# Kernel tuning notes

Hardware: AMD Instinct MI355X
Metric: run time of the kernel (lower is better)

Reference implementation:

```python
import jax, jax.numpy as jnp
import numpy as np

D_MODEL = 768
NUM_HEADS = 12
HEAD_DIM = D_MODEL // NUM_HEADS  # 64, also rotary dim
INTERMEDIATE = 1152
WINDOW = 128          # config.local_attention (layer_id=1 -> local layer)
ROPE_BASE = 10000.0   # local_rope_theta
EPS = 1e-5


def layer_norm_nocenter(x, gamma):
    # keras LayerNormalization(center=False): mean-subtract, no beta
    mu = jnp.mean(x, axis=-1, keepdims=True)
    var = jnp.var(x, axis=-1, keepdims=True)
    return (x - mu) * jax.lax.rsqrt(var + EPS) * gamma


def rotate_half(x):
    x1, x2 = jnp.split(x, 2, axis=-1)
    return jnp.concatenate([-x2, x1], axis=-1)


def setup_inputs() -> dict:
    key = jax.random.key(0)
    ks = jax.random.split(key, 7)
    B, S = 4, 2048
    hidden_states = jax.random.normal(ks[0], (B, S, D_MODEL), dtype=jnp.float32)
    attention_mask = jnp.zeros((B, 1, S, S), dtype=jnp.float32)  # no padding
    s = 0.02
    attn_norm_gamma = jnp.ones((D_MODEL,), dtype=jnp.float32)
    wqkv = jax.random.normal(ks[1], (D_MODEL, 3 * D_MODEL), dtype=jnp.float32) * s
    wo_attn = jax.random.normal(ks[2], (D_MODEL, D_MODEL), dtype=jnp.float32) * s
    mlp_norm_gamma = jnp.ones((D_MODEL,), dtype=jnp.float32)
    wi = jax.random.normal(ks[3], (D_MODEL, 2 * INTERMEDIATE), dtype=jnp.float32) * s
    wo_mlp = jax.random.normal(ks[4], (INTERMEDIATE, D_MODEL), dtype=jnp.float32) * s
    return {
        'hidden_states': hidden_states,
        'attention_mask': attention_mask,
        'attn_norm_gamma': attn_norm_gamma,
        'wqkv': wqkv,
        'wo_attn': wo_attn,
        'mlp_norm_gamma': mlp_norm_gamma,
        'wi': wi,
        'wo_mlp': wo_mlp,
    }


def reference(hidden_states, attention_mask, attn_norm_gamma, wqkv, wo_attn,
              mlp_norm_gamma, wi, wo_mlp):
    B, S, Dm = hidden_states.shape
    H, Dh = NUM_HEADS, HEAD_DIM

    # RoPE cache (NTKScaling with scaling_factor=1 -> plain RoPE)
    idx = jnp.arange(0, Dh, 2, dtype=jnp.float32)
    inv_freq = 1.0 / (ROPE_BASE ** (idx / Dh))          # [Dh/2]
    t = jnp.arange(S, dtype=jnp.float32)
    freqs = t[:, None] * inv_freq[None, :]              # [S, Dh/2]
    emb = jnp.concatenate([freqs, freqs], axis=-1)      # [S, Dh]
    cos = jnp.cos(emb)[None, None]                      # [1,1,S,Dh]
    sin = jnp.sin(emb)[None, None]

    # combined sliding-window + padding mask
    pos = jnp.arange(S)
    dist = jnp.abs(pos[:, None] - pos[None, :])
    neg = jnp.finfo(jnp.float32).min
    local = jnp.where(dist <= WINDOW // 2, 0.0, neg).astype(jnp.float32)
    mask = attention_mask + local[None, None]           # [B,1,S,S]

    # attention (layer_id != 0 -> pre-norm)
    x = layer_norm_nocenter(hidden_states, attn_norm_gamma)
    qkv = (x @ wqkv).reshape(B, S, 3, H, Dh).transpose(2, 0, 3, 1, 4)
    q, k, v = qkv[0], qkv[1], qkv[2]                    # [B,H,S,Dh]
    q = q * cos + rotate_half(q) * sin
    k = k * cos + rotate_half(k) * sin

    scale = 1.0 / jnp.sqrt(jnp.asarray(Dh, q.dtype))
    scores = jnp.einsum('bhqd,bhkd->bhqk', q, k) * scale + mask
    attn = jax.nn.softmax(scores, axis=-1)
    ctx = jnp.einsum('bhqk,bhkd->bhqd', attn, v)
    attn_out = ctx.transpose(0, 2, 1, 3).reshape(B, S, Dm) @ wo_attn

    h = hidden_states + attn_out

    # GLU MLP: Wi -> split -> gelu(x)*gate -> Wo, residual
    n = layer_norm_nocenter(h, mlp_norm_gamma)
    x_in, gate = jnp.split(n @ wi, 2, axis=-1)
    mlp = jax.nn.gelu(x_in, approximate=False) * gate
    return h + mlp @ wo_mlp
```

## Files before the change

### kernel.cpp

```cpp
#include <hip/hip_runtime.h>
#include <cstdint>
#include <cstddef>

typedef __bf16 bf16;
typedef float f32x4 __attribute__((ext_vector_type(4)));
typedef __bf16 bf16x8 __attribute__((ext_vector_type(8)));
typedef __bf16 bf16x4 __attribute__((ext_vector_type(4)));

#define MFMA16(a, b, c) __builtin_amdgcn_mfma_f32_16x16x32_bf16((a), (b), (c), 0, 0, 0)

__device__ __forceinline__ void gload_lds16(const void* g, void* l) {
  __builtin_amdgcn_global_load_lds((__attribute__((address_space(1))) void*)g,
                                   (__attribute__((address_space(3))) void*)l,
                                   16, 0, 0);
}

__global__ __launch_bounds__(256) void wconv_kernel(const float* __restrict__ W,
                                                    bf16* __restrict__ Wt, int K, int N) {
  __shared__ float tile[32][33];
  const int n0 = blockIdx.x * 32, k0 = blockIdx.y * 32;
  const int t = threadIdx.x;
  const int c = t & 31, r = t >> 5;
#pragma unroll
  for (int i = 0; i < 4; ++i)
    tile[r + i * 8][c] = W[(size_t)(k0 + r + i * 8) * N + n0 + c];
  __syncthreads();
#pragma unroll
  for (int i = 0; i < 4; ++i)
    Wt[(size_t)(n0 + r + i * 8) * K + k0 + c] = (bf16)tile[c][r + i * 8];
}

__global__ __launch_bounds__(256) void ln_kernel(const float* __restrict__ X,
                                                 const float* __restrict__ gamma,
                                                 bf16* __restrict__ out) {
  const int row = blockIdx.x, t = threadIdx.x;
  const float* xr = X + (size_t)row * 768;
  float v0 = xr[t], v1 = xr[t + 256], v2 = xr[t + 512];
  float s = v0 + v1 + v2;
  float s2 = v0 * v0 + v1 * v1 + v2 * v2;
#pragma unroll
  for (int m = 1; m <= 32; m <<= 1) {
    s += __shfl_xor(s, m, 64);
    s2 += __shfl_xor(s2, m, 64);
  }
  __shared__ float red[8];
  const int w = t >> 6, lane = t & 63;
  if (lane == 0) { red[w] = s; red[4 + w] = s2; }
  __syncthreads();
  s = red[0] + red[1] + red[2] + red[3];
  s2 = red[4] + red[5] + red[6] + red[7];
  const float mu = s * (1.f / 768.f);
  const float var = s2 * (1.f / 768.f) - mu * mu;
  const float rs = rsqrtf(var + 1e-5f);
  out[(size_t)row * 768 + t] = (bf16)((v0 - mu) * rs * gamma[t]);
  out[(size_t)row * 768 + t + 256] = (bf16)((v1 - mu) * rs * gamma[t + 256]);
  out[(size_t)row * 768 + t + 512] = (bf16)((v2 - mu) * rs * gamma[t + 512]);
}

template <int BM, bool RES, typename TOUT>
__global__ __launch_bounds__(256) void gemm_bt(const bf16* __restrict__ A,
                                               const bf16* __restrict__ Bt,
                                               const float* __restrict__ Res,
                                               TOUT* __restrict__ C, int M, int N, int K) {
  constexpr int MT = BM / 32;
  __shared__ __align__(16) bf16 As[BM * 64];
  __shared__ __align__(16) bf16 Bs[128 * 64];
  const int t = threadIdx.x;
  const int lane = t & 63;
  const int w = t >> 6;
  const int wm = w >> 1, wn = w & 1;
  const int row0 = blockIdx.y * BM, col0 = blockIdx.x * 128;
  const int rm = lane & 15, qd = lane >> 4;
  f32x4 acc[MT][4] = {};
  for (int k0 = 0; k0 < K; k0 += 64) {
#pragma unroll
    for (int i = 0; i < BM / 32; ++i) {
      int c = i * 256 + t;
      int r = c >> 3, j = (c & 7) ^ (r & 7);
      gload_lds16(A + (size_t)(row0 + r) * K + (k0 + j * 8), &As[c * 8]);
    }
#pragma unroll
    for (int i = 0; i < 4; ++i) {
      int c = i * 256 + t;
      int r = c >> 3, j = (c & 7) ^ (r & 7);
      gload_lds16(Bt + (size_t)(col0 + r) * K + (k0 + j * 8), &Bs[c * 8]);
    }
    __syncthreads();
#pragma unroll
    for (int kb = 0; kb < 2; ++kb) {
      bf16x8 af[MT], bfr[4];
#pragma unroll
      for (int mt = 0; mt < MT; ++mt) {
        int r = wm * (MT * 16) + mt * 16 + rm;
        af[mt] = *(const bf16x8*)&As[r * 64 + (((kb * 4 + qd) ^ (r & 7)) * 8)];
      }
#pragma unroll
      for (int nt = 0; nt < 4; ++nt) {
        int r = wn * 64 + nt * 16 + rm;
        bfr[nt] = *(const bf16x8*)&Bs[r * 64 + (((kb * 4 + qd) ^ (r & 7)) * 8)];
      }
#pragma unroll
      for (int mt = 0; mt < MT; ++mt)
#pragma unroll
        for (int nt = 0; nt < 4; ++nt)
          acc[mt][nt] = MFMA16(af[mt], bfr[nt], acc[mt][nt]);
    }
    __syncthreads();
  }
#pragma unroll
  for (int mt = 0; mt < MT; ++mt)
#pragma unroll
    for (int nt = 0; nt < 4; ++nt) {
      const int gc = col0 + wn * 64 + nt * 16 + rm;
#pragma unroll
      for (int r = 0; r < 4; ++r) {
        const int gr = row0 + wm * (MT * 16) + mt * 16 + qd * 4 + r;
        float v = acc[mt][nt][r];
        const size_t idx = (size_t)gr * N + gc;
        if (RES) v += Res[idx];
        C[idx] = (TOUT)v;
      }
    }
}

__global__ __launch_bounds__(256) void gemm_qkv(const bf16* __restrict__ A,
                                                const bf16* __restrict__ Bt,
                                                bf16* __restrict__ Qb,
                                                bf16* __restrict__ Kb,
                                                bf16* __restrict__ Vt) {
  __shared__ __align__(16) bf16 As[128 * 64];
  __shared__ __align__(16) bf16 Bs[128 * 64];
  const int t = threadIdx.x;
  const int lane = t & 63;
  const int w = t >> 6;
  const int wm = w >> 1, wn = w & 1;
  const int row0 = blockIdx.y * 128, col0 = blockIdx.x * 128;
  const int rm = lane & 15, qd = lane >> 4;
  f32x4 acc[4][4] = {};
  for (int k0 = 0; k0 < 768; k0 += 64) {
#pragma unroll
    for (int i = 0; i < 4; ++i) {
      int c = i * 256 + t;
      int r = c >> 3, j = (c & 7) ^ (r & 7);
      gload_lds16(A + (size_t)(row0 + r) * 768 + (k0 + j * 8), &As[c * 8]);
      int c2 = i * 256 + t;
      gload_lds16(Bt + (size_t)(col0 + r) * 768 + (k0 + j * 8), &Bs[c2 * 8]);
    }
    __syncthreads();
#pragma unroll
    for (int kb = 0; kb < 2; ++kb) {
      bf16x8 af[4], bfr[4];
#pragma unroll
      for (int mt = 0; mt < 4; ++mt) {
        int r = wm * 64 + mt * 16 + rm;
        af[mt] = *(const bf16x8*)&As[r * 64 + (((kb * 4 + qd) ^ (r & 7)) * 8)];
      }
#pragma unroll
      for (int nt = 0; nt < 4; ++nt) {
        int r = wn * 64 + nt * 16 + rm;
        bfr[nt] = *(const bf16x8*)&Bs[r * 64 + (((kb * 4 + qd) ^ (r & 7)) * 8)];
      }
#pragma unroll
      for (int mt = 0; mt < 4; ++mt)
#pragma unroll
        for (int nt = 0; nt < 4; ++nt)
          acc[mt][nt] = MFMA16(af[mt], bfr[nt], acc[mt][nt]);
    }
    __syncthreads();
  }

  const int head_id = blockIdx.x * 2 + wn;
  const int typ = head_id / 12;
  const int h = head_id - typ * 12;
  const int b = row0 >> 11;
  const int sw = (row0 & 2047) + wm * 64;
  const size_t bhbase = (size_t)(b * 12 + h) * 2048;

  if (typ < 2) {
    bf16* dst = typ ? Kb : Qb;
    float invf[2];
#pragma unroll
    for (int nt = 0; nt < 2; ++nt)
      invf[nt] = exp2f((float)(nt * 16 + rm) * -0.41524101186092029f);
#pragma unroll
    for (int mt = 0; mt < 4; ++mt)
#pragma unroll
      for (int r = 0; r < 4; ++r) {
        int s = sw + mt * 16 + qd * 4 + r;
#pragma unroll
        for (int nt = 0; nt < 2; ++nt) {
          float ang = (float)s * invf[nt];
          float rev = ang * 0.15915494309189535f;
          rev -= floorf(rev);
          float sn = __builtin_amdgcn_sinf(rev);
          float cs = __builtin_amdgcn_cosf(rev);
          float x1 = acc[mt][nt][r], x2 = acc[mt][nt + 2][r];
          int d = nt * 16 + rm;
          dst[(bhbase + s) * 64 + d] = (bf16)(x1 * cs - x2 * sn);
          dst[(bhbase + s) * 64 + d + 32] = (bf16)(x2 * cs + x1 * sn);
        }
      }
  } else {
#pragma unroll
    for (int mt = 0; mt < 4; ++mt)
#pragma unroll
      for (int nt = 0; nt < 4; ++nt) {
        int d = nt * 16 + rm;
        int s4 = sw + mt * 16 + qd * 4;
        bf16x4 v4;
#pragma unroll
        for (int r = 0; r < 4; ++r) v4[r] = (bf16)acc[mt][nt][r];
        *(bf16x4*)&Vt[(bhbase * 64) + ((size_t)(h * 0) ) + ((size_t)( (b * 12 + h) * 64 + d)) * 2048 + s4 - bhbase * 64] = v4;
      }
  }
}

__global__ __launch_bounds__(256) void gemm_wi_geglu(const bf16* __restrict__ A,
                                                     const bf16* __restrict__ Bt,
                                                     bf16* __restrict__ outp) {
  __shared__ __align__(16) bf16 As[128 * 64];
  __shared__ __align__(16) bf16 Bxs[64 * 64];
  __shared__ __align__(16) bf16 Bgs[64 * 64];
  const int t = threadIdx.x;
  const int lane = t & 63;
  const int w = t >> 6;
  const int wm = w >> 1, wn = w & 1;
  const int row0 = blockIdx.y * 128, col0 = blockIdx.x * 64;
  const int rm = lane & 15, qd = lane >> 4;
  f32x4 accx[4][2] = {}, accg[4][2] = {};
  for (int k0 = 0; k0 < 768; k0 += 64) {
#pragma unroll
    for (int i = 0; i < 4; ++i) {
      int c = i * 256 + t;
      int r = c >> 3, j = (c & 7) ^ (r & 7);
      gload_lds16(A + (size_t)(row0 + r) * 768 + (k0 + j * 8), &As[c * 8]);
    }
#pragma unroll
    for (int i = 0; i < 2; ++i) {
      int c = i * 256 + t;
      int r = c >> 3, j = (c & 7) ^ (r & 7);
      gload_lds16(Bt + (size_t)(col0 + r) * 768 + (k0 + j * 8), &Bxs[c * 8]);
      gload_lds16(Bt + (size_t)(1152 + col0 + r) * 768 + (k0 + j * 8), &Bgs[c * 8]);
    }
    __syncthreads();
#pragma unroll
    for (int kb = 0; kb < 2; ++kb) {
      bf16x8 af[4], bx[2], bg[2];
#pragma unroll
      for (int mt = 0; mt < 4; ++mt) {
        int r = wm * 64 + mt * 16 + rm;
        af[mt] = *(const bf16x8*)&As[r * 64 + (((kb * 4 + qd) ^ (r & 7)) * 8)];
      }
#pragma unroll
      for (int nt = 0; nt < 2; ++nt) {
        int r = wn * 32 + nt * 16 + rm;
        int off = r * 64 + (((kb * 4 + qd) ^ (r & 7)) * 8);
        bx[nt] = *(const bf16x8*)&Bxs[off];
        bg[nt] = *(const bf16x8*)&Bgs[off];
      }
#pragma unroll
      for (int mt = 0; mt < 4; ++mt)
#pragma unroll
        for (int nt = 0; nt < 2; ++nt) {
          accx[mt][nt] = MFMA16(af[mt], bx[nt], accx[mt][nt]);
          accg[mt][nt] = MFMA16(af[mt], bg[nt], accg[mt][nt]);
        }
    }
    __syncthreads();
  }
#pragma unroll
  for (int mt = 0; mt < 4; ++mt)
#pragma unroll
    for (int nt = 0; nt < 2; ++nt) {
      const int gc = col0 + wn * 32 + nt * 16 + rm;
#pragma unroll
      for (int r = 0; r < 4; ++r) {
        const int gr = row0 + wm * 64 + mt * 16 + qd * 4 + r;
        float x = accx[mt][nt][r], g = accg[mt][nt][r];
        float ge = 0.5f * x * (1.0f + erff(x * 0.70710678118654752f));
        outp[(size_t)gr * 1152 + gc] = (bf16)(ge * g);
      }
    }
}

__global__ __launch_bounds__(256) void attn_kernel(const bf16* __restrict__ Qb,
                                                   const bf16* __restrict__ Kb,
                                                   const bf16* __restrict__ Vt,
                                                   const float* __restrict__ am,
                                                   bf16* __restrict__ ctx) {
  __shared__ __align__(16) bf16 KP[64 * 200];
  __shared__ __align__(16) bf16 Vts[64 * 192];
  bf16* Ks = KP;
  bf16* Ps = KP;

  const int t = threadIdx.x;
  const int lane = t & 63, w = t >> 6;
  const int rm = lane & 15, qd = lane >> 4;
  const int s0 = blockIdx.x * 64;
  const int bh = blockIdx.y;
  const int b = bh / 12, h = bh - b * 12;
  const size_t baseQ = (size_t)bh * 2048;

#pragma unroll
  for (int i = 0; i < 6; ++i) {
    int c = i * 256 + t;
    int r = c >> 3, j = (c & 7) ^ (r & 7);
    int key = min(max(s0 - 64 + r, 0), 2047);
    gload_lds16(Kb + (baseQ + key) * 64 + j * 8, &Ks[c * 8]);
  }
#pragma unroll
  for (int i = 0; i < 6; ++i) {
    int c = i * 256 + t;
    int r = c / 24, jl = c - r * 24;
    int j = (jl & 24) | ((jl & 7) ^ (r & 7));
    int k0 = min(max(s0 - 64 + j * 8, 0), 2040);
    gload_lds16(Vt + ((size_t)bh * 64 + r) * 2048 + k0, &Vts[c * 8]);
  }

  bf16x8 aq[2];
#pragma unroll
  for (int kb = 0; kb < 2; ++kb)
    aq[kb] = *(const bf16x8*)&Qb[(baseQ + s0 + w * 16 + rm) * 64 + kb * 32 + qd * 8];

  float msk[12][4];
#pragma unroll
  for (int nt = 0; nt < 12; ++nt) {
    int key = s0 - 64 + nt * 16 + rm;
#pragma unroll
    for (int r = 0; r < 4; ++r) {
      int qpos = s0 + w * 16 + qd * 4 + r;
      bool valid = (key >= 0) && (key < 2048) && (key - qpos <= 64) && (qpos - key <= 64);
      msk[nt][r] = valid ? am[((size_t)b * 2048 + qpos) * 2048 + key] : -3e38f;
    }
  }
  __syncthreads();

  f32x4 sc[12];
#pragma unroll
  for (int nt = 0; nt < 12; ++nt) {
    f32x4 a = {0.f, 0.f, 0.f, 0.f};
#pragma unroll
    for (int kb = 0; kb < 2; ++kb) {
      int r = nt * 16 + rm;
      bf16x8 bk = *(const bf16x8*)&Ks[r * 64 + (((kb * 4 + qd) ^ (rm & 7)) * 8)];
      a = MFMA16(aq[kb], bk, a);
    }
    sc[nt] = a;
  }

  float mx[4] = {-3e38f, -3e38f, -3e38f, -3e38f};
#pragma unroll
  for (int nt = 0; nt < 12; ++nt)
#pragma unroll
    for (int r = 0; r < 4; ++r) {
      float v = (msk[nt][r] <= -2.9e38f) ? -3e38f : sc[nt][r] * 0.125f + msk[nt][r];
      sc[nt][r] = v;
      mx[r] = fmaxf(mx[r], v);
    }
#pragma unroll
  for (int r = 0; r < 4; ++r)
#pragma unroll
    for (int m = 1; m <= 8; m <<= 1) mx[r] = fmaxf(mx[r], __shfl_xor(mx[r], m, 64));
  float sum[4] = {0.f, 0.f, 0.f, 0.f};
#pragma unroll
  for (int nt = 0; nt < 12; ++nt)
#pragma unroll
    for (int r = 0; r < 4; ++r) {
      float p = (sc[nt][r] > -1e37f) ? __expf(sc[nt][r] - mx[r]) : 0.f;
      sc[nt][r] = p;
      sum[r] += p;
    }
#pragma unroll
  for (int r = 0; r < 4; ++r)
#pragma unroll
    for (int m = 1; m <= 8; m <<= 1) sum[r] += __shfl_xor(sum[r], m, 64);
  float inv[4];
#pragma unroll
  for (int r = 0; r < 4; ++r) inv[r] = 1.f / sum[r];

  __syncthreads();

#pragma unroll
  for (int nt = 0; nt < 12; ++nt)
#pragma unroll
    for (int r = 0; r < 4; ++r)
      Ps[(w * 16 + qd * 4 + r) * 200 + nt * 16 + rm] = (bf16)(sc[nt][r] * inv[r]);

  f32x4 o[4] = {};
#pragma unroll
  for (int ks = 0; ks < 6; ++ks) {
    bf16x8 ap = *(const bf16x8*)&Ps[(w * 16 + rm) * 200 + ks * 32 + qd * 8];
#pragma unroll
    for (int nt = 0; nt < 4; ++nt) {
      int kc = ks * 4 + qd;
      bf16x8 bv = *(const bf16x8*)&Vts[(nt * 16 + rm) * 192 +
                                       (((kc & 24) | ((kc & 7) ^ (rm & 7))) * 8)];
      o[nt] = MFMA16(ap, bv, o[nt]);
    }
  }
#pragma unroll
  for (int nt = 0; nt < 4; ++nt)
#pragma unroll
    for (int r = 0; r < 4; ++r) {
      int q_ = s0 + w * 16 + qd * 4 + r;
      ctx[((size_t)(b * 2048 + q_)) * 768 + h * 64 + nt * 16 + rm] = (bf16)o[nt][r];
    }
}

extern "C" void kernel_launch(void* const* d_in, const int* in_sizes, int n_in,
                              void* d_out, int out_size, void* d_ws, size_t ws_size,
                              hipStream_t stream) {
  (void)in_sizes; (void)n_in; (void)out_size; (void)ws_size;
  const float* hidden = (const float*)d_in[0];
  const float* amask = (const float*)d_in[1];
  const float* g1 = (const float*)d_in[2];
  const float* wqkv = (const float*)d_in[3];
  const float* woa = (const float*)d_in[4];
  const float* g2 = (const float*)d_in[5];
  const float* wi = (const float*)d_in[6];
  const float* wom = (const float*)d_in[7];
  float* out = (float*)d_out;

  char* p = (char*)d_ws;
  size_t o = 0;
  auto take = [&](size_t bytes) {
    char* r = p + o;
    o = (o + bytes + 255) & ~(size_t)255;
    return r;
  };
  bf16* wqkvT = (bf16*)take((size_t)2304 * 768 * 2);
  bf16* woaT = (bf16*)take((size_t)768 * 768 * 2);
  bf16* wiT = (bf16*)take((size_t)2304 * 768 * 2);
  bf16* womT = (bf16*)take((size_t)768 * 1152 * 2);
  bf16* xn = (bf16*)take((size_t)8192 * 768 * 2);
  bf16* Qb = (bf16*)take((size_t)98304 * 64 * 2);
  bf16* Kb = (bf16*)take((size_t)98304 * 64 * 2);
  bf16* Vt = (bf16*)take((size_t)98304 * 64 * 2);
  bf16* ctxb = (bf16*)take((size_t)8192 * 768 * 2);
  float* hbuf = (float*)take((size_t)8192 * 768 * 4);
  bf16* mlp = (bf16*)take((size_t)8192 * 1152 * 2);

  wconv_kernel<<<dim3(72, 24), 256, 0, stream>>>(wqkv, wqkvT, 768, 2304);
  wconv_kernel<<<dim3(24, 24), 256, 0, stream>>>(woa, woaT, 768, 768);
  wconv_kernel<<<dim3(72, 24), 256, 0, stream>>>(wi, wiT, 768, 2304);
  wconv_kernel<<<dim3(24, 36), 256, 0, stream>>>(wom, womT, 1152, 768);

  ln_kernel<<<8192, 256, 0, stream>>>(hidden, g1, xn);
  gemm_qkv<<<dim3(18, 64), 256, 0, stream>>>(xn, wqkvT, Qb, Kb, Vt);
  attn_kernel<<<dim3(32, 48), 256, 0, stream>>>(Qb, Kb, Vt, amask, ctxb);
  gemm_bt<64, true, float><<<dim3(6, 128), 256, 0, stream>>>(ctxb, woaT, hidden, hbuf,
                                                             8192, 768, 768);

  ln_kernel<<<8192, 256, 0, stream>>>(hbuf, g2, xn);
  gemm_wi_geglu<<<dim3(18, 64), 256, 0, stream>>>(xn, wiT, mlp);
  gemm_bt<64, true, float><<<dim3(6, 128), 256, 0, stream>>>(mlp, womT, hbuf, out,
                                                             8192, 768, 1152);
}
```

Before: 329.5 us.

## Interleave Wi columns for GEGLU, stage V transpose via LDS, merge weight conversion

```diff
diff --git a/kernel.cpp b/kernel.cpp
--- a/kernel.cpp
+++ b/kernel.cpp
@@ -15,10 +15,26 @@
                                    16, 0, 0);
 }
 
-__global__ __launch_bounds__(256) void wconv_kernel(const float* __restrict__ W,
-                                                    bf16* __restrict__ Wt, int K, int N) {
+__global__ __launch_bounds__(256) void wconv_all(const float* __restrict__ wqkv,
+                                                 const float* __restrict__ woa,
+                                                 const float* __restrict__ wi,
+                                                 const float* __restrict__ wom,
+                                                 bf16* __restrict__ wqkvT,
+                                                 bf16* __restrict__ woaT,
+                                                 bf16* __restrict__ wiIT,
+                                                 bf16* __restrict__ womT) {
+  int id = blockIdx.x;
+  const float* W;
+  bf16* Wt;
+  int K, N, bx, by;
+  bool inter = false;
+  if (id < 1728) { W = wqkv; Wt = wqkvT; K = 768; N = 2304; bx = id % 72; by = id / 72; }
+  else if (id < 2304) { id -= 1728; W = woa; Wt = woaT; K = 768; N = 768; bx = id % 24; by = id / 24; }
+  else if (id < 4032) { id -= 2304; W = wi; Wt = wiIT; K = 768; N = 2304; inter = true; bx = id % 72; by = id / 72; }
+  else { id -= 4032; W = wom; Wt = womT; K = 1152; N = 768; bx = id % 24; by = id / 24; }
+
   __shared__ float tile[32][33];
-  const int n0 = blockIdx.x * 32, k0 = blockIdx.y * 32;
+  const int n0 = bx * 32, k0 = by * 32;
   const int t = threadIdx.x;
   const int c = t & 31, r = t >> 5;
 #pragma unroll
@@ -26,8 +42,11 @@
     tile[r + i * 8][c] = W[(size_t)(k0 + r + i * 8) * N + n0 + c];
   __syncthreads();
 #pragma unroll
-  for (int i = 0; i < 4; ++i)
-    Wt[(size_t)(n0 + r + i * 8) * K + k0 + c] = (bf16)tile[c][r + i * 8];
+  for (int i = 0; i < 4; ++i) {
+    int n = n0 + r + i * 8;
+    int nw = inter ? ((n < 1152) ? 2 * n : 2 * (n - 1152) + 1) : n;
+    Wt[(size_t)nw * K + k0 + c] = (bf16)tile[c][r + i * 8];
+  }
 }
 
 __global__ __launch_bounds__(256) void ln_kernel(const float* __restrict__ X,
@@ -123,11 +142,9 @@
     }
 }
 
-__global__ __launch_bounds__(256) void gemm_qkv(const bf16* __restrict__ A,
-                                                const bf16* __restrict__ Bt,
-                                                bf16* __restrict__ Qb,
-                                                bf16* __restrict__ Kb,
-                                                bf16* __restrict__ Vt) {
+__global__ __launch_bounds__(256) void gemm_wi(const bf16* __restrict__ A,
+                                               const bf16* __restrict__ Bt,
+                                               bf16* __restrict__ outp) {
   __shared__ __align__(16) bf16 As[128 * 64];
   __shared__ __align__(16) bf16 Bs[128 * 64];
   const int t = threadIdx.x;
@@ -143,8 +160,7 @@
       int c = i * 256 + t;
       int r = c >> 3, j = (c & 7) ^ (r & 7);
       gload_lds16(A + (size_t)(row0 + r) * 768 + (k0 + j * 8), &As[c * 8]);
-      int c2 = i * 256 + t;
-      gload_lds16(Bt + (size_t)(col0 + r) * 768 + (k0 + j * 8), &Bs[c2 * 8]);
+      gload_lds16(Bt + (size_t)(col0 + r) * 768 + (k0 + j * 8), &Bs[c * 8]);
     }
     __syncthreads();
 #pragma unroll
@@ -168,15 +184,81 @@
     }
     __syncthreads();
   }
+#pragma unroll
+  for (int mt = 0; mt < 4; ++mt)
+#pragma unroll
+    for (int nt = 0; nt < 4; ++nt) {
+      const int ci = col0 + wn * 64 + nt * 16 + rm;
+#pragma unroll
+      for (int r = 0; r < 4; ++r) {
+        const int gr = row0 + wm * 64 + mt * 16 + qd * 4 + r;
+        float v = acc[mt][nt][r];
+        float other = __shfl_xor(v, 1, 64);
+        if ((rm & 1) == 0) {
+          float x = v, g = other;
+          float ge = 0.5f * x * (1.0f + erff(x * 0.70710678118654752f));
+          outp[(size_t)gr * 1152 + (ci >> 1)] = (bf16)(ge * g);
+        }
+      }
+    }
+}
+
+__global__ __launch_bounds__(256) void gemm_qkv(const bf16* __restrict__ A,
+                                                const bf16* __restrict__ Bt,
+                                                bf16* __restrict__ Qb,
+                                                bf16* __restrict__ Kb,
+                                                bf16* __restrict__ Vt) {
+  __shared__ __align__(16) bf16 SM[17408];
+  bf16* As = SM;
+  bf16* Bs = SM + 8192;
+
+  const int t = threadIdx.x;
+  const int lane = t & 63;
+  const int w = t >> 6;
+  const int wm = w >> 1, wn = w & 1;
+  const int row0 = blockIdx.y * 128, col0 = blockIdx.x * 128;
+  const int rm = lane & 15, qd = lane >> 4;
+  f32x4 acc[4][4] = {};
+  for (int k0 = 0; k0 < 768; k0 += 64) {
+#pragma unroll
+    for (int i = 0; i < 4; ++i) {
+      int c = i * 256 + t;
+      int r = c >> 3, j = (c & 7) ^ (r & 7);
+      gload_lds16(A + (size_t)(row0 + r) * 768 + (k0 + j * 8), &As[c * 8]);
+      gload_lds16(Bt + (size_t)(col0 + r) * 768 + (k0 + j * 8), &Bs[c * 8]);
+    }
+    __syncthreads();
+#pragma unroll
+    for (int kb = 0; kb < 2; ++kb) {
+      bf16x8 af[4], bfr[4];
+#pragma unroll
+      for (int mt = 0; mt < 4; ++mt) {
+        int r = wm * 64 + mt * 16 + rm;
+        af[mt] = *(const bf16x8*)&As[r * 64 + (((kb * 4 + qd) ^ (r & 7)) * 8)];
+      }
+#pragma unroll
+      for (int nt = 0; nt < 4; ++nt) {
+        int r = wn * 64 + nt * 16 + rm;
+        bfr[nt] = *(const bf16x8*)&Bs[r * 64 + (((kb * 4 + qd) ^ (r & 7)) * 8)];
+      }
+#pragma unroll
+      for (int mt = 0; mt < 4; ++mt)
+#pragma unroll
+        for (int nt = 0; nt < 4; ++nt)
+          acc[mt][nt] = MFMA16(af[mt], bfr[nt], acc[mt][nt]);
+    }
+    __syncthreads();
+  }
 
   const int head_id = blockIdx.x * 2 + wn;
-  const int typ = head_id / 12;
-  const int h = head_id - typ * 12;
+  const int typ = blockIdx.x / 6;
   const int b = row0 >> 11;
-  const int sw = (row0 & 2047) + wm * 64;
-  const size_t bhbase = (size_t)(b * 12 + h) * 2048;
+  const int sblk = row0 & 2047;
+  const int sw = sblk + wm * 64;
 
   if (typ < 2) {
+    const int h = head_id - typ * 12;
+    const size_t bhbase = (size_t)(b * 12 + h) * 2048;
     bf16* dst = typ ? Kb : Qb;
     float invf[2];
 #pragma unroll
@@ -205,82 +287,24 @@
     for (int mt = 0; mt < 4; ++mt)
 #pragma unroll
       for (int nt = 0; nt < 4; ++nt) {
-        int d = nt * 16 + rm;
-        int s4 = sw + mt * 16 + qd * 4;
+        int hd = wn * 64 + nt * 16 + rm;
+        int sl = wm * 64 + mt * 16 + qd * 4;
         bf16x4 v4;
 #pragma unroll
         for (int r = 0; r < 4; ++r) v4[r] = (bf16)acc[mt][nt][r];
-        *(bf16x4*)&Vt[(bhbase * 64) + ((size_t)(h * 0) ) + ((size_t)( (b * 12 + h) * 64 + d)) * 2048 + s4 - bhbase * 64] = v4;
-      }
-  }
-}
-
-__global__ __launch_bounds__(256) void gemm_wi_geglu(const bf16* __restrict__ A,
-                                                     const bf16* __restrict__ Bt,
-                                                     bf16* __restrict__ outp) {
-  __shared__ __align__(16) bf16 As[128 * 64];
-  __shared__ __align__(16) bf16 Bxs[64 * 64];
-  __shared__ __align__(16) bf16 Bgs[64 * 64];
-  const int t = threadIdx.x;
-  const int lane = t & 63;
-  const int w = t >> 6;
-  const int wm = w >> 1, wn = w & 1;
-  const int row0 = blockIdx.y * 128, col0 = blockIdx.x * 64;
-  const int rm = lane & 15, qd = lane >> 4;
-  f32x4 accx[4][2] = {}, accg[4][2] = {};
-  for (int k0 = 0; k0 < 768; k0 += 64) {
-#pragma unroll
-    for (int i = 0; i < 4; ++i) {
-      int c = i * 256 + t;
-      int r = c >> 3, j = (c & 7) ^ (r & 7);
-      gload_lds16(A + (size_t)(row0 + r) * 768 + (k0 + j * 8), &As[c * 8]);
-    }
-#pragma unroll
-    for (int i = 0; i < 2; ++i) {
-      int c = i * 256 + t;
-      int r = c >> 3, j = (c & 7) ^ (r & 7);
-      gload_lds16(Bt + (size_t)(col0 + r) * 768 + (k0 + j * 8), &Bxs[c * 8]);
-      gload_lds16(Bt + (size_t)(1152 + col0 + r) * 768 + (k0 + j * 8), &Bgs[c * 8]);
-    }
-    __syncthreads();
-#pragma unroll
-    for (int kb = 0; kb < 2; ++kb) {
-      bf16x8 af[4], bx[2], bg[2];
-#pragma unroll
-      for (int mt = 0; mt < 4; ++mt) {
-        int r = wm * 64 + mt * 16 + rm;
-        af[mt] = *(const bf16x8*)&As[r * 64 + (((kb * 4 + qd) ^ (r & 7)) * 8)];
-      }
-#pragma unroll
-      for (int nt = 0; nt < 2; ++nt) {
-        int r = wn * 32 + nt * 16 + rm;
-        int off = r * 64 + (((kb * 4 + qd) ^ (r & 7)) * 8);
-        bx[nt] = *(const bf16x8*)&Bxs[off];
-        bg[nt] = *(const bf16x8*)&Bgs[off];
-      }
-#pragma unroll
-      for (int mt = 0; mt < 4; ++mt)
-#pragma unroll
-        for (int nt = 0; nt < 2; ++nt) {
-          accx[mt][nt] = MFMA16(af[mt], bx[nt], accx[mt][nt]);
-          accg[mt][nt] = MFMA16(af[mt], bg[nt], accg[mt][nt]);
-        }
-    }
-    __syncthreads();
-  }
-#pragma unroll
-  for (int mt = 0; mt < 4; ++mt)
-#pragma unroll
-    for (int nt = 0; nt < 2; ++nt) {
-      const int gc = col0 + wn * 32 + nt * 16 + rm;
-#pragma unroll
-      for (int r = 0; r < 4; ++r) {
-        const int gr = row0 + wm * 64 + mt * 16 + qd * 4 + r;
-        float x = accx[mt][nt][r], g = accg[mt][nt][r];
-        float ge = 0.5f * x * (1.0f + erff(x * 0.70710678118654752f));
-        outp[(size_t)gr * 1152 + gc] = (bf16)(ge * g);
-      }
-    }
+        *(bf16x4*)&SM[hd * 136 + sl] = v4;
+      }
+    __syncthreads();
+    const int h0 = blockIdx.x * 2 - 24;
+#pragma unroll
+    for (int it = 0; it < 8; ++it) {
+      int cc = it * 256 + t;
+      int hd = cc >> 4, s8 = (cc & 15) * 8;
+      bf16x8 vv = *(const bf16x8*)&SM[hd * 136 + s8];
+      size_t grow = (size_t)(b * 12 + h0 + (hd >> 6)) * 64 + (hd & 63);
+      *(bf16x8*)&Vt[grow * 2048 + sblk + s8] = vv;
+    }
+  }
 }
 
 __global__ __launch_bounds__(256) void attn_kernel(const bf16* __restrict__ Qb,
@@ -430,7 +454,7 @@
   };
   bf16* wqkvT = (bf16*)take((size_t)2304 * 768 * 2);
   bf16* woaT = (bf16*)take((size_t)768 * 768 * 2);
-  bf16* wiT = (bf16*)take((size_t)2304 * 768 * 2);
+  bf16* wiIT = (bf16*)take((size_t)2304 * 768 * 2);
   bf16* womT = (bf16*)take((size_t)768 * 1152 * 2);
   bf16* xn = (bf16*)take((size_t)8192 * 768 * 2);
   bf16* Qb = (bf16*)take((size_t)98304 * 64 * 2);
@@ -440,10 +464,7 @@
   float* hbuf = (float*)take((size_t)8192 * 768 * 4);
   bf16* mlp = (bf16*)take((size_t)8192 * 1152 * 2);
 
-  wconv_kernel<<<dim3(72, 24), 256, 0, stream>>>(wqkv, wqkvT, 768, 2304);
-  wconv_kernel<<<dim3(24, 24), 256, 0, stream>>>(woa, woaT, 768, 768);
-  wconv_kernel<<<dim3(72, 24), 256, 0, stream>>>(wi, wiT, 768, 2304);
-  wconv_kernel<<<dim3(24, 36), 256, 0, stream>>>(wom, womT, 1152, 768);
+  wconv_all<<<4896, 256, 0, stream>>>(wqkv, woa, wi, wom, wqkvT, woaT, wiIT, womT);
 
   ln_kernel<<<8192, 256, 0, stream>>>(hidden, g1, xn);
   gemm_qkv<<<dim3(18, 64), 256, 0, stream>>>(xn, wqkvT, Qb, Kb, Vt);
@@ -452,7 +473,7 @@
                                                              8192, 768, 768);
 
   ln_kernel<<<8192, 256, 0, stream>>>(hbuf, g2, xn);
-  gemm_wi_geglu<<<dim3(18, 64), 256, 0, stream>>>(xn, wiT, mlp);
+  gemm_wi<<<dim3(18, 64), 256, 0, stream>>>(xn, wiIT, mlp);
   gemm_bt<64, true, float><<<dim3(6, 128), 256, 0, stream>>>(mlp, womT, hbuf, out,
                                                              8192, 768, 1152);
 }
```

After: 342.7 us. 1.04x slower.
